# Optimization experiments

Measured on AMD Instinct MI355X. Metric: run time of the kernel, lower is better.

The kernel has to match this reference:

```python
import jax, jax.numpy as jnp
import numpy as np

ALPHA = 0.001
TAU = 1.0
KAPPA = 1.0
N_ITER = 1


def setup_inputs() -> dict:
    key = jax.random.key(0)
    k1, k2, k3, k4, k5 = jax.random.split(key, 5)
    B, H, N, K = 8, 8, 512, 16
    mu = jax.random.normal(k1, (B, N, K), dtype=jnp.float32)
    # beta: softmax-like attention weights over j (positive, rows sum to 1)
    beta = jax.nn.softmax(jax.random.normal(k2, (B, H, N, N), dtype=jnp.float32), axis=-1)
    mu_prior = jax.random.normal(k3, (B, N, K), dtype=jnp.float32)
    phi = 0.1 * jax.random.normal(k4, (B, N, 3), dtype=jnp.float32)
    g = jax.random.normal(k5, (3, K, K), dtype=jnp.float32)
    generators = 0.5 * (g - jnp.swapaxes(g, -1, -2))  # skew-symmetric so(3) rep -> stable expm
    lr = jnp.asarray(0.05, dtype=jnp.float32)
    return {"mu": mu, "beta": beta, "mu_prior": mu_prior, "phi": phi,
            "generators": generators, "lr": lr}


def _transport(mu, phi, generators):
    # phi_algebra[b,n] = sum_g phi[b,n,g] * G_g  -> (B,N,K,K)
    B, N, K = mu.shape
    phi_alg = jnp.einsum('bng,gkl->bnkl', phi, generators)
    expm = jax.vmap(jax.scipy.linalg.expm)
    Om_i = expm(phi_alg.reshape(B * N, K, K)).reshape(B, N, K, K)
    Om_j_inv = expm((-phi_alg).reshape(B * N, K, K)).reshape(B, N, K, K)
    # mu_t[b,i,j] = Om_i[b,i] @ (Om_j_inv[b,j] @ mu[b,j])  (factored, avoids (B,N,N,K,K))
    v = jnp.einsum('bjlm,bjm->bjl', Om_j_inv, mu)          # (B,N,K)
    mu_t = jnp.einsum('bikl,bjl->bijk', Om_i, v)           # (B,N,N,K)
    return mu_t


def reference(mu, beta, mu_prior, phi, generators, lr):
    beta_avg = beta.mean(axis=1)                           # (B,N,N)
    mu_cur = mu
    for _ in range(N_ITER):
        grad_prior = ALPHA * (mu_cur - mu_prior)
        mu_t = _transport(mu_cur, phi, generators)         # (B,N,N,K)
        delta = mu_cur[:, :, None, :] - mu_t               # (B,N,N,K)
        # TERM 1: sum_j (beta_ij/tau) * delta_ij
        grad1 = jnp.einsum('bij,bijk->bik', beta_avg, delta) / TAU
        # TERM 2 (second-order): sum_j sum_k (beta_ij/kappa)(delta_jk - beta_ik) KL_ij gkl_ik
        #   = (1/kappa)[ sum_j beta_ij KL_ij gkl_ij - (sum_j beta_ij KL_ij) * sum_k beta_ik gkl_ik ]
        kl = jnp.sum(delta * delta, axis=-1) / (2.0 * TAU)  # (B,N,N)
        gkl = delta / TAU                                   # (B,N,N,K)
        w = beta_avg * kl                                   # (B,N,N)
        term1 = jnp.einsum('bij,bijk->bik', w, gkl)
        s = jnp.sum(w, axis=-1)                             # (B,N)
        bsum = jnp.einsum('bij,bijk->bik', beta_avg, gkl)
        grad2 = (term1 - s[..., None] * bsum) / KAPPA
        mu_cur = mu_cur - lr * (grad_prior + grad1 + grad2)
    return mu_cur
```

## Files before the change

### kernel.cpp

```cpp
#include <hip/hip_runtime.h>
#include <hip/hip_bf16.h>
#include <cstddef>
#include <cstdint>

#define B_ 8
#define H_ 8
#define N_ 512
#define K_ 16
#define NN_ (N_*N_)

static constexpr float ALPHA_C = 0.001f;

typedef float f32x4 __attribute__((ext_vector_type(4)));

#define LDSTRIDE 20

__device__ __forceinline__ void mm_rowB(const float* a, const float* Bbuf,
                                        int c0, f32x4& acc)
{
    #pragma unroll
    for (int k = 0; k < 16; ++k) {
        const f32x4 bk = *(const f32x4*)&Bbuf[k * LDSTRIDE + c0];
        acc.x = fmaf(a[k], bk.x, acc.x);
        acc.y = fmaf(a[k], bk.y, acc.y);
        acc.z = fmaf(a[k], bk.z, acc.z);
        acc.w = fmaf(a[k], bk.w, acc.w);
    }
}

__device__ __forceinline__ void read_row(const float* buf, int r, float* a)
{
    #pragma unroll
    for (int i = 0; i < 4; ++i) {
        const f32x4 t = *(const f32x4*)&buf[r * LDSTRIDE + 4 * i];
        a[4*i]   = t.x; a[4*i+1] = t.y; a[4*i+2] = t.z; a[4*i+3] = t.w;
    }
}

__device__ __forceinline__ void write_strip(float* buf, int r, int c0, f32x4 s)
{
    *(f32x4*)&buf[r * LDSTRIDE + c0] = s;
}

__global__ __launch_bounds__(256) void expm_kernel(
    const float* __restrict__ mu, const float* __restrict__ phi,
    const float* __restrict__ gen, float* __restrict__ Om,
    float* __restrict__ v, float* __restrict__ q)
{
    __shared__ float lds[4][2][16 * LDSTRIDE];

    const int tid  = threadIdx.x;
    const int w    = tid >> 6, lane = tid & 63;
    const int r    = lane >> 2, c0 = (lane & 3) << 2;
    const int bn   = (blockIdx.x << 2) | w;

    float* U0 = lds[w][0];
    float* U1 = lds[w][1];

    const float p0 = phi[bn*3+0], p1 = phi[bn*3+1], p2 = phi[bn*3+2];
    const int gidx = r * 16 + c0;
    const f32x4 g0 = *(const f32x4*)&gen[gidx];
    const f32x4 g1 = *(const f32x4*)&gen[256 + gidx];
    const f32x4 g2 = *(const f32x4*)&gen[512 + gidx];
    f32x4 As;
    As.x = p0*g0.x + p1*g1.x + p2*g2.x;
    As.y = p0*g0.y + p1*g1.y + p2*g2.y;
    As.z = p0*g0.z + p1*g1.z + p2*g2.z;
    As.w = p0*g0.w + p1*g1.w + p2*g2.w;

    float t = As.x*As.x + As.y*As.y + As.z*As.z + As.w*As.w;
    #pragma unroll
    for (int m = 1; m <= 32; m <<= 1) t += __shfl_xor(t, m, 64);
    float theta = sqrtf(t);
    int s = 0;
    while (theta > 1.0f && s < 30) { theta *= 0.5f; ++s; }
    const float sc = exp2f((float)(-s));
    const f32x4 Xs = As * sc;

    write_strip(U0, r, c0, Xs);
    float xrow[16];
    read_row(U0, r, xrow);

    f32x4 a2s = {0.f, 0.f, 0.f, 0.f};
    mm_rowB(xrow, U0, c0, a2s);
    write_strip(U1, r, c0, a2s);

    f32x4 a3s = {0.f, 0.f, 0.f, 0.f};
    mm_rowB(xrow, U1, c0, a3s);

    float a2row[16];
    read_row(U1, r, a2row);
    f32x4 a4s = {0.f, 0.f, 0.f, 0.f};
    mm_rowB(a2row, U1, c0, a4s);
    write_strip(U0, r, c0, a4s);
    float a4row[16];
    read_row(U0, r, a4row);

    f32x4 di = {0.f, 0.f, 0.f, 0.f};
    if (r >= c0 && r < c0 + 4) ((float*)&di)[r - c0] = 1.0f;

    const f32x4 C0 = di + Xs + a2s * 0.5f + a3s * (1.0f/6.0f);
    const f32x4 C1 = di * (1.0f/24.0f) + Xs * (1.0f/120.0f)
                   + a2s * (1.0f/720.0f) + a3s * (1.0f/5040.0f);
    const f32x4 Q2 = di * (1.0f/40320.0f) + Xs * (1.0f/362880.0f)
                   + a2s * (1.0f/3628800.0f) + a3s * (1.0f/39916800.0f)
                   + a4s * (1.0f/479001600.0f);

    write_strip(U1, r, c0, Q2);
    f32x4 T1 = C1;
    mm_rowB(a4row, U1, c0, T1);

    write_strip(U1, r, c0, T1);
    f32x4 P = C0;
    mm_rowB(a4row, U1, c0, P);

    for (int it = 0; it < s; ++it) {
        write_strip(U1, r, c0, P);
        float prow[16];
        read_row(U1, r, prow);
        f32x4 Pn = {0.f, 0.f, 0.f, 0.f};
        mm_rowB(prow, U1, c0, Pn);
        P = Pn;
    }

    *(f32x4*)&Om[(size_t)bn * 256 + r * 16 + c0] = P;

    const float mur = mu[bn * 16 + r];
    f32x4 vc = P * mur;
    #pragma unroll
    for (int m = 4; m <= 32; m <<= 1) {
        vc.x += __shfl_xor(vc.x, m, 64);
        vc.y += __shfl_xor(vc.y, m, 64);
        vc.z += __shfl_xor(vc.z, m, 64);
        vc.w += __shfl_xor(vc.w, m, 64);
    }
    if (r == 0) *(f32x4*)&v[bn * 16 + c0] = vc;

    float qp = vc.x*vc.x + vc.y*vc.y + vc.z*vc.z + vc.w*vc.w;
    qp += __shfl_xor(qp, 1, 64);
    qp += __shfl_xor(qp, 2, 64);
    if (lane == 0) q[bn] = 0.5f * qp;
}

__global__ __launch_bounds__(256, 4) void grad_kernel(
    const float* __restrict__ mu, const float* __restrict__ beta,
    const float* __restrict__ mu_prior, const float* __restrict__ lrp,
    const float* __restrict__ Om, const float* __restrict__ v,
    const float* __restrict__ q, float* __restrict__ out)
{
    __shared__ float v_t[16 * 516];
    __shared__ f32x4 q4[128];

    const int blk = blockIdx.x;
    const int b   = blk >> 7;
    const int i0  = (blk & 127) << 2;
    const int tid = threadIdx.x;
    const int wid = tid >> 6, lane = tid & 63;

    const float* vb = v + (size_t)b * N_ * K_;
    for (int f = tid; f < N_ * K_; f += 256) {
        const int j = f >> 4, k = f & 15;
        v_t[k * 516 + j] = vb[f];
    }
    const f32x4* qb4 = (const f32x4*)(q + (size_t)b * N_);
    if (tid < 128) q4[tid] = qb4[tid];
    __syncthreads();

    const int i = i0 + wid;

    float vi[16];
    #pragma unroll
    for (int k = 0; k < 16; ++k) vi[k] = v_t[k * 516 + i];
    const float qi = ((const float*)q4)[i];

    float w1[16], w2[16];
    #pragma unroll
    for (int k = 0; k < 16; ++k) { w1[k] = 0.f; w2[k] = 0.f; }
    float sacc = 0.f, R = 0.f;

    const size_t betaBase = (((size_t)b * H_) * N_ + i) * N_;

    #pragma unroll 1
    for (int p = 0; p < 2; ++p) {
        const int j0 = (lane << 2) | (p << 8);

        const float* bp = beta + betaBase + j0;
        float rx = 0.f, ry = 0.f, rz = 0.f, rw = 0.f;
        #pragma unroll
        for (int h = 0; h < H_; ++h) {
            const f32x4 bt = __builtin_nontemporal_load(
                (const f32x4*)(bp + (size_t)h * NN_));
            rx += bt.x; ry += bt.y; rz += bt.z; rw += bt.w;
        }
        rx *= 0.125f; ry *= 0.125f; rz *= 0.125f; rw *= 0.125f;

        float d0 = 0.f, d1 = 0.f, d2 = 0.f, d3 = 0.f;
        #pragma unroll
        for (int k = 0; k < 16; ++k) {
            const f32x4 vj = *(const f32x4*)&v_t[k * 516 + j0];
            d0 = fmaf(vi[k], vj.x, d0);
            d1 = fmaf(vi[k], vj.y, d1);
            d2 = fmaf(vi[k], vj.z, d2);
            d3 = fmaf(vi[k], vj.w, d3);
        }
        const f32x4 qj = q4[lane | (p << 6)];
        const float rkl0 = rx * (qi + qj.x - d0);
        const float rkl1 = ry * (qi + qj.y - d1);
        const float rkl2 = rz * (qi + qj.z - d2);
        const float rkl3 = rw * (qi + qj.w - d3);
        sacc += (rkl0 + rkl1) + (rkl2 + rkl3);
        R    += (rx + ry) + (rz + rw);

        #pragma unroll
        for (int k = 0; k < 16; ++k) {
            const f32x4 vj = *(const f32x4*)&v_t[k * 516 + j0];
            float a1 = fmaf(rx, vj.x, w1[k]);
            a1 = fmaf(ry, vj.y, a1);
            a1 = fmaf(rz, vj.z, a1);
            w1[k] = fmaf(rw, vj.w, a1);
            float a2 = fmaf(rkl0, vj.x, w2[k]);
            a2 = fmaf(rkl1, vj.y, a2);
            a2 = fmaf(rkl2, vj.z, a2);
            w2[k] = fmaf(rkl3, vj.w, a2);
        }
    }

    #pragma unroll
    for (int off = 32; off > 0; off >>= 1) {
        #pragma unroll
        for (int k = 0; k < 16; ++k) {
            w1[k] += __shfl_xor(w1[k], off, 64);
            w2[k] += __shfl_xor(w2[k], off, 64);
        }
        sacc += __shfl_xor(sacc, off, 64);
        R    += __shfl_xor(R,    off, 64);
    }

    float gvec[16];
    #pragma unroll
    for (int k = 0; k < 16; ++k)
        gvec[k] = (1.0f - sacc) * (R * vi[k] - w1[k]) + sacc * vi[k] - w2[k];

    if (lane < 16) {
        const float lr = lrp[0];
        const size_t rowi = (size_t)b * N_ + i;
        const float* omr = Om + rowi * 256 + (size_t)lane * 16;
        float S = 0.f;
        #pragma unroll
        for (int c2 = 0; c2 < 16; ++c2) S = fmaf(omr[c2], gvec[c2], S);
        const size_t oi = rowi * 16 + lane;
        const float m0 = mu[oi], mp = mu_prior[oi];
        out[oi] = m0 - lr * (ALPHA_C * (m0 - mp) + S);
    }
}

extern "C" void kernel_launch(void* const* d_in, const int* in_sizes, int n_in,
                              void* d_out, int out_size, void* d_ws, size_t ws_size,
                              hipStream_t stream)
{
    const float* mu   = (const float*)d_in[0];
    const float* beta = (const float*)d_in[1];
    const float* mup  = (const float*)d_in[2];
    const float* phi  = (const float*)d_in[3];
    const float* gen  = (const float*)d_in[4];
    const float* lr   = (const float*)d_in[5];
    float* out = (float*)d_out;

    float* Om = (float*)d_ws;
    float* v  = Om + (size_t)4096 * 256;
    float* q  = v  + (size_t)4096 * 16;

    expm_kernel<<<B_ * N_ / 4, 256, 0, stream>>>(mu, phi, gen, Om, v, q);
    grad_kernel<<<B_ * (N_ / 4), 256, 0, stream>>>(mu, beta, mup, lr, Om, v, q, out);
}
```

Before: 135.6 us.

## Use transpose-reduce across lanes for gradient vectors and raise expm scaling threshold

The final reduction of the 32 per-lane accumulators (w1, w2) switches from a full butterfly shuffle per element to a recursive-halving transpose-reduce. The two accumulators are first folded into one vector, so each lane ends up owning one component. The Om-times-gradient product is then spread across all 64 lanes with a similar reduction, and the v staging loads become float4. The expm scaling threshold rises from 1 to 2, which cuts squarings but leaves the degree-12 Taylor approximation with a larger norm, at some accuracy risk.

```diff
diff --git a/kernel.cpp b/kernel.cpp
--- a/kernel.cpp
+++ b/kernel.cpp
@@ -73,7 +73,7 @@
     for (int m = 1; m <= 32; m <<= 1) t += __shfl_xor(t, m, 64);
     float theta = sqrtf(t);
     int s = 0;
-    while (theta > 1.0f && s < 30) { theta *= 0.5f; ++s; }
+    while (theta > 2.0f && s < 30) { theta *= 0.5f; ++s; }
     const float sc = exp2f((float)(-s));
     const f32x4 Xs = As * sc;
 
@@ -158,9 +158,14 @@
     const int wid = tid >> 6, lane = tid & 63;
 
     const float* vb = v + (size_t)b * N_ * K_;
-    for (int f = tid; f < N_ * K_; f += 256) {
-        const int j = f >> 4, k = f & 15;
-        v_t[k * 516 + j] = vb[f];
+    for (int f4 = tid; f4 < (N_ * K_) / 4; f4 += 256) {
+        const f32x4 tq = *(const f32x4*)&vb[f4 << 2];
+        const int j  = f4 >> 2;
+        const int k0 = (f4 & 3) << 2;
+        v_t[(k0+0) * 516 + j] = tq.x;
+        v_t[(k0+1) * 516 + j] = tq.y;
+        v_t[(k0+2) * 516 + j] = tq.z;
+        v_t[(k0+3) * 516 + j] = tq.w;
     }
     const f32x4* qb4 = (const f32x4*)(q + (size_t)b * N_);
     if (tid < 128) q4[tid] = qb4[tid];
@@ -227,30 +232,81 @@
 
     #pragma unroll
     for (int off = 32; off > 0; off >>= 1) {
-        #pragma unroll
-        for (int k = 0; k < 16; ++k) {
-            w1[k] += __shfl_xor(w1[k], off, 64);
-            w2[k] += __shfl_xor(w2[k], off, 64);
-        }
         sacc += __shfl_xor(sacc, off, 64);
         R    += __shfl_xor(R,    off, 64);
     }
-
-    float gvec[16];
-    #pragma unroll
-    for (int k = 0; k < 16; ++k)
-        gvec[k] = (1.0f - sacc) * (R * vi[k] - w1[k]) + sacc * vi[k] - w2[k];
+    const float oms  = 1.0f - sacc;
+    const float coef = oms * R + sacc;
+
+    float wc[16];
+    #pragma unroll
+    for (int k = 0; k < 16; ++k) wc[k] = fmaf(oms, w1[k], w2[k]);
+
+    {
+        #pragma unroll
+        for (int k = 0; k < 8; ++k) {
+            const bool up = (lane & 32) != 0;
+            const float send = up ? wc[k] : wc[k + 8];
+            const float recv = __shfl_xor(send, 32, 64);
+            wc[k] = (up ? wc[k + 8] : wc[k]) + recv;
+        }
+        #pragma unroll
+        for (int k = 0; k < 4; ++k) {
+            const bool up = (lane & 16) != 0;
+            const float send = up ? wc[k] : wc[k + 4];
+            const float recv = __shfl_xor(send, 16, 64);
+            wc[k] = (up ? wc[k + 4] : wc[k]) + recv;
+        }
+        #pragma unroll
+        for (int k = 0; k < 2; ++k) {
+            const bool up = (lane & 8) != 0;
+            const float send = up ? wc[k] : wc[k + 2];
+            const float recv = __shfl_xor(send, 8, 64);
+            wc[k] = (up ? wc[k + 2] : wc[k]) + recv;
+        }
+        {
+            const bool up = (lane & 4) != 0;
+            const float send = up ? wc[0] : wc[1];
+            const float recv = __shfl_xor(send, 4, 64);
+            wc[0] = (up ? wc[1] : wc[0]) + recv;
+        }
+        wc[0] += __shfl_xor(wc[0], 2, 64);
+        wc[0] += __shfl_xor(wc[0], 1, 64);
+    }
+
+    const int cmine = (lane >> 2) & 15;
+    const float gv = coef * v_t[cmine * 516 + i] - wc[0];
+
+    const size_t rowi = (size_t)b * N_ + i;
+    const float* omb = Om + rowi * 256;
+    const int tq = lane & 3;
+    float pr[4];
+    #pragma unroll
+    for (int rr = 0; rr < 4; ++rr)
+        pr[rr] = omb[(4 * tq + rr) * 16 + cmine] * gv;
+
+    #pragma unroll
+    for (int k = 0; k < 2; ++k) {
+        const bool up = (lane & 4) != 0;
+        const float send = up ? pr[k] : pr[k + 2];
+        const float recv = __shfl_xor(send, 4, 64);
+        pr[k] = (up ? pr[k + 2] : pr[k]) + recv;
+    }
+    {
+        const bool up = (lane & 8) != 0;
+        const float send = up ? pr[0] : pr[1];
+        const float recv = __shfl_xor(send, 8, 64);
+        pr[0] = (up ? pr[1] : pr[0]) + recv;
+    }
+    pr[0] += __shfl_xor(pr[0], 16, 64);
+    pr[0] += __shfl_xor(pr[0], 32, 64);
 
     if (lane < 16) {
+        const int row = 4 * tq + 2 * ((lane >> 2) & 1) + ((lane >> 3) & 1);
         const float lr = lrp[0];
-        const size_t rowi = (size_t)b * N_ + i;
-        const float* omr = Om + rowi * 256 + (size_t)lane * 16;
-        float S = 0.f;
-        #pragma unroll
-        for (int c2 = 0; c2 < 16; ++c2) S = fmaf(omr[c2], gvec[c2], S);
-        const size_t oi = rowi * 16 + lane;
+        const size_t oi = rowi * 16 + row;
         const float m0 = mu[oi], mp = mu_prior[oi];
-        out[oi] = m0 - lr * (ALPHA_C * (m0 - mp) + S);
+        out[oi] = m0 - lr * (ALPHA_C * (m0 - mp) + pr[0]);
     }
 }
 
```

After: 133.9 us. About the same (-1.3%).
